# Kernel optimization log

Hardware: AMD Instinct MI355X
Metric: run time of the kernel (lower is better)

Reference implementation:

```python
import jax, jax.numpy as jnp
import numpy as np

NUM_HEADS = 16
HIDDEN = 1024
HEAD_DIM = HIDDEN // NUM_HEADS
B, L = 1, 2048


def setup_inputs() -> dict:
    key = jax.random.key(0)
    ks = jax.random.split(key, 5)
    scale = 1.0 / np.sqrt(HIDDEN)
    x = jax.random.normal(ks[0], (B, L, HIDDEN), dtype=jnp.float32)
    Wq = jax.random.normal(ks[1], (HIDDEN, HIDDEN), dtype=jnp.float32) * scale
    Wk = jax.random.normal(ks[2], (HIDDEN, HIDDEN), dtype=jnp.float32) * scale
    Wv = jax.random.normal(ks[3], (HIDDEN, HIDDEN), dtype=jnp.float32) * scale
    Wo = jax.random.normal(ks[4], (HIDDEN, HIDDEN), dtype=jnp.float32) * scale
    return {"x": x, "Wq": Wq, "Wk": Wk, "Wv": Wv, "Wo": Wo}


def reference(x, Wq, Wk, Wv, Wo):
    Bx, Lx, _ = x.shape
    # nn.Linear computes x @ W.T (bias=False)
    q = (x @ Wq.T).reshape(Bx, Lx, NUM_HEADS, HEAD_DIM)
    k = (x @ Wk.T).reshape(Bx, Lx, NUM_HEADS, HEAD_DIM)
    v = (x @ Wv.T).reshape(Bx, Lx, NUM_HEADS, HEAD_DIM)
    # elu(.)+1 feature map
    q = jax.nn.elu(q) + 1.0
    k = jax.nn.elu(k) + 1.0
    # causal linear-attention state via cumsum of kv outer products
    kv = jnp.einsum('blhd,blhe->blhde', k, v)           # [B,L,H,D,D]
    kv_cumsum = jnp.cumsum(kv, axis=1)
    k_cumsum = jnp.cumsum(k, axis=1)
    out = jnp.einsum('blhd,blhde->blhe', q, kv_cumsum)   # [B,L,H,D]
    denom = jnp.clip(jnp.einsum('blhd,blhd->blh', q, k_cumsum), 1e-6, None)
    out = out / denom[..., None]
    return out.reshape(Bx, Lx, HIDDEN) @ Wo.T
```

## Files before the change

### kernel.cpp

```cpp
#include <hip/hip_runtime.h>
#include <hip/hip_bf16.h>

typedef __attribute__((ext_vector_type(8))) short short8;
typedef __attribute__((ext_vector_type(4))) float floatx4;
typedef __attribute__((ext_vector_type(8))) unsigned short ushortx8;
typedef __attribute__((ext_vector_type(4))) unsigned short ushortx4;
typedef unsigned short u16;

#define HIDDEN 1024
#define NH 16
#define HD 64
#define SEQ 2048
#define CHUNK 128
#define NCHUNK (SEQ / CHUNK)

__device__ __forceinline__ u16 f2bf(float f) {
    union { float f; unsigned u; } v; v.f = f;
    unsigned r = v.u + 0x7fffu + ((v.u >> 16) & 1u);
    return (u16)(r >> 16);
}
__device__ __forceinline__ float bf2f(u16 u) {
    union { unsigned u; float f; } v; v.u = ((unsigned)u) << 16;
    return v.f;
}

__device__ __forceinline__ void gl_lds16(const u16* g, u16* l) {
    __builtin_amdgcn_global_load_lds(
        (const __attribute__((address_space(1))) void*)g,
        (__attribute__((address_space(3))) void*)l,
        16, 0, 0);
}

__global__ __launch_bounds__(256)
void convert_all(const float* __restrict__ x,  const float* __restrict__ Wq,
                 const float* __restrict__ Wk, const float* __restrict__ Wv,
                 const float* __restrict__ Wo,
                 u16* __restrict__ xb, u16* __restrict__ Wb, u16* __restrict__ Wob)
{
    const int total4 = 1572864;
    for (int idx = blockIdx.x * 256 + threadIdx.x; idx < total4; idx += gridDim.x * 256) {
        const float4* src; u16* dst; int off;
        if (idx < 524288)       { src = (const float4*)x;  dst = xb;            off = idx; }
        else if (idx < 786432)  { src = (const float4*)Wq; dst = Wb;            off = idx - 524288; }
        else if (idx < 1048576) { src = (const float4*)Wk; dst = Wb + 1048576;  off = idx - 786432; }
        else if (idx < 1310720) { src = (const float4*)Wv; dst = Wb + 2097152;  off = idx - 1048576; }
        else                    { src = (const float4*)Wo; dst = Wob;           off = idx - 1310720; }
        float4 v = src[off];
        ushortx4 u = { f2bf(v.x), f2bf(v.y), f2bf(v.z), f2bf(v.w) };
        *(ushortx4*)(dst + (size_t)off * 4) = u;
    }
}

__global__ __launch_bounds__(256, 3)
void qkv_gemm64(const u16* __restrict__ A, const u16* __restrict__ Bm,
                u16* __restrict__ qkb, u16* __restrict__ kT_b, u16* __restrict__ vT_b)
{
    __shared__ __align__(16) u16 smem[24576];
    auto As = (u16(*)[4096])smem;
    auto Bs = (u16(*)[8192])(smem + 8192);
    u16* Trow = smem;
    u16* Tcol = smem + 8704;

    const int L = blockIdx.x;
    const int xc = L & 7, i5 = L >> 3;
    const int m0 = (((xc >> 2) * 16) + (i5 & 15)) * 64;
    const int n0 = (((xc & 3) * 6) + (i5 >> 4)) * 128;

    const int t = threadIdx.x;
    const int lane = t & 63, wave = t >> 6;
    const int ln = lane & 15, q4 = lane >> 4;
    const int wm = (wave >> 1) * 32, wn = (wave & 1) * 64;
    const int r_in = t >> 3;
    const int csw = (((t & 7) ^ (r_in & 7)) << 3);

    const u16* Ag = A + (size_t)(m0 + r_in) * 1024 + csw;
    const u16* Bg = Bm + (size_t)(n0 + r_in) * 1024 + csw;

    floatx4 acc[2][4];
#pragma unroll
    for (int i = 0; i < 2; i++)
#pragma unroll
        for (int j = 0; j < 4; j++) acc[i][j] = (floatx4)0.0f;

    auto stage = [&](int buf, int k) {
        const int k0 = k * 64;
        gl_lds16(Ag + k0, &As[buf][t * 8]);
        gl_lds16(Ag + k0 + 32 * 1024, &As[buf][2048 + t * 8]);
#pragma unroll
        for (int i = 0; i < 4; i++)
            gl_lds16(Bg + k0 + (size_t)i * 32 * 1024, &Bs[buf][i * 2048 + t * 8]);
    };
    auto compute = [&](int buf) {
#pragma unroll
        for (int s = 0; s < 2; s++) {
            const int rc = (((s * 4 + q4) ^ (ln & 7)) << 3);
            short8 af[2], bfr[4];
#pragma unroll
            for (int i = 0; i < 2; i++)
                af[i] = *(const short8*)&As[buf][(wm + i * 16 + ln) * 64 + rc];
#pragma unroll
            for (int j = 0; j < 4; j++)
                bfr[j] = *(const short8*)&Bs[buf][(wn + j * 16 + ln) * 64 + rc];
#pragma unroll
            for (int i = 0; i < 2; i++)
#pragma unroll
                for (int j = 0; j < 4; j++)
                    acc[i][j] = __builtin_amdgcn_mfma_f32_16x16x32_bf16(af[i], bfr[j], acc[i][j], 0, 0, 0);
        }
    };

    stage(0, 0);
    stage(1, 1);
    for (int i = 0; i < 14; i++) {
        asm volatile("s_waitcnt vmcnt(6)" ::: "memory");
        __builtin_amdgcn_sched_barrier(0);
        __builtin_amdgcn_s_barrier();
        compute(i & 1);
        __builtin_amdgcn_sched_barrier(0);
        __builtin_amdgcn_s_barrier();
        stage(i & 1, i + 2);
    }
    asm volatile("s_waitcnt vmcnt(6)" ::: "memory");
    __builtin_amdgcn_sched_barrier(0);
    __builtin_amdgcn_s_barrier();
    compute(0);
    asm volatile("s_waitcnt vmcnt(0)" ::: "memory");
    __builtin_amdgcn_sched_barrier(0);
    __builtin_amdgcn_s_barrier();
    compute(1);

    __syncthreads();
    const int grp = n0 >> 10;
#pragma unroll
    for (int i = 0; i < 2; i++)
#pragma unroll
        for (int j = 0; j < 4; j++) {
            const int ml = wm + i * 16 + q4 * 4;
            const int nl = wn + j * 16 + ln;
            float vals[4];
#pragma unroll
            for (int r = 0; r < 4; r++) {
                float v = acc[i][j][r];
                if (grp < 2) v = (v > 0.f) ? (v + 1.f) : __expf(v);
                vals[r] = v;
            }
            if (grp < 2) {
#pragma unroll
                for (int r = 0; r < 4; r++) Trow[(ml + r) * 136 + nl] = f2bf(vals[r]);
            }
            if (grp >= 1) {
                ushortx4 u = { f2bf(vals[0]), f2bf(vals[1]), f2bf(vals[2]), f2bf(vals[3]) };
                *(ushortx4*)&Tcol[nl * 72 + ml] = u;
            }
        }
    __syncthreads();
    if (grp < 2) {
        const int ml = t >> 2, sg = (t & 3) * 32;
        const int col0 = (n0 & 1023) + (grp ? 1024 : 0) + sg;
        const u16* src = &Trow[ml * 136 + sg];
        u16* dst = &qkb[(size_t)(m0 + ml) * 2048 + col0];
#pragma unroll
        for (int p = 0; p < 4; p++)
            *(ushortx8*)&dst[p * 8] = *(const ushortx8*)&src[p * 8];
    }
    if (grp >= 1) {
        const int nl = t >> 1, sg = (t & 1) * 32;
        const int nh = (n0 & 1023) + nl;
        const u16* src = &Tcol[nl * 72 + sg];
        u16* dstb = (grp == 1) ? kT_b : vT_b;
        u16* dst = &dstb[(size_t)nh * 2048 + m0 + sg];
#pragma unroll
        for (int p = 0; p < 4; p++)
            *(ushortx8*)&dst[p * 8] = *(const ushortx8*)&src[p * 8];
    }
}

__global__ __launch_bounds__(256, 2)
void chunk_stats2(const u16* __restrict__ kT_b, const u16* __restrict__ vT_b,
                  float* __restrict__ S_ws, float* __restrict__ ksum_ws)
{
    __shared__ u16 kT_l[64 * 128];
    __shared__ u16 vT_l[64 * 128];
    const int c = blockIdx.x, h = blockIdx.y;
    const int t = threadIdx.x;
    const int lane = t & 63, w = t >> 6;
    const int ln = lane & 15, q4 = lane >> 4;
#pragma unroll
    for (int i = 0; i < 4; i++) {
        const int d0 = w * 16 + i * 4 + (lane >> 4);
        const int cc = lane & 15;
        const size_t gsrc = (size_t)(h * 64 + d0) * 2048 + c * 128 + ((cc ^ (d0 & 7)) << 3);
        gl_lds16(kT_b + gsrc, &kT_l[(w * 16 + i * 4) * 128 + lane * 8]);
        gl_lds16(vT_b + gsrc, &vT_l[(w * 16 + i * 4) * 128 + lane * 8]);
    }
    __syncthreads();
    floatx4 sacc[4];
#pragma unroll
    for (int j = 0; j < 4; j++) sacc[j] = (floatx4)0.0f;
#pragma unroll
    for (int ks = 0; ks < 4; ks++) {
        const int rc = (((ks * 4 + q4) ^ (ln & 7)) << 3);
        short8 af = *(const short8*)&kT_l[(w * 16 + ln) * 128 + rc];
#pragma unroll
        for (int j = 0; j < 4; j++) {
            short8 bfr = *(const short8*)&vT_l[(j * 16 + ln) * 128 + rc];
            sacc[j] = __builtin_amdgcn_mfma_f32_16x16x32_bf16(af, bfr, sacc[j], 0, 0, 0);
        }
    }
    float* Sp = S_ws + ((size_t)(h * NCHUNK + c) << 12);
#pragma unroll
    for (int j = 0; j < 4; j++)
#pragma unroll
        for (int r = 0; r < 4; r++) {
            int d = w * 16 + q4 * 4 + r;
            int e = j * 16 + ln;
            Sp[e * 64 + d] = sacc[j][r];
        }
    if (t < 64) {
        float s = 0.f;
#pragma unroll
        for (int cc = 0; cc < 16; cc++) {
            ushortx8 v8 = *(const ushortx8*)&kT_l[t * 128 + cc * 8];
#pragma unroll
            for (int jj = 0; jj < 8; jj++) s += bf2f(v8[jj]);
        }
        ksum_ws[(h * NCHUNK + c) * 64 + t] = s;
    }
}

__global__ __launch_bounds__(256)
void scan_kv(const float* __restrict__ S_ws, const float* __restrict__ ksum_ws,
             u16* __restrict__ kvpref_b, float* __restrict__ kspref)
{
    const int h = blockIdx.x, qt = blockIdx.y;
    const int t = threadIdx.x;
    const int li = qt * 1024 + t * 4;
    const int e = li >> 6, d0 = li & 63;
    const int slot = e * 64 + ((((d0 >> 3) ^ (e & 7)) << 3) | (d0 & 7));
    float a0 = 0.f, a1 = 0.f, a2 = 0.f, a3 = 0.f;
    for (int c = 0; c < 16; c++) {
        ushortx4 u = { f2bf(a0), f2bf(a1), f2bf(a2), f2bf(a3) };
        *(ushortx4*)&kvpref_b[(((size_t)(h * 16 + c)) << 12) + slot] = u;
        float4 s4 = *(const float4*)(S_ws + (((size_t)(h * 16 + c)) << 12) + li);
        a0 += s4.x; a1 += s4.y; a2 += s4.z; a3 += s4.w;
    }
    if (qt == 0 && t < 64) {
        float a = 0.f;
        for (int c = 0; c < 16; c++) {
            kspref[(h * 16 + c) * 64 + t] = a;
            a += ksum_ws[(h * 16 + c) * 64 + t];
        }
    }
}

__global__ __launch_bounds__(512, 2)
void attn_out2(const u16* __restrict__ qkb, const u16* __restrict__ vT_b,
               const u16* __restrict__ kvpref_b, const float* __restrict__ kspref,
               u16* __restrict__ attnb)
{
    __shared__ __align__(16) u16 smem[29824];
    u16* q_l   = smem;
    u16* k_l   = smem + 8192;
    u16* kvT_l = smem + 16384;
    u16* vT_l  = smem + 20480;
    u16* P_l   = smem;
    float* kpref  = (float*)(smem + 28672);
    float* denom4 = kpref + 64;

    const int c = blockIdx.x, h = blockIdx.y;
    const int t = threadIdx.x;
    const int lane = t & 63, w = t >> 6;
    const int ln = lane & 15, q4 = lane >> 4;

    {
        const int row = t >> 3, cc = t & 7;
        const size_t gq = (size_t)(c * CHUNK + row) * 2048 + h * 64
                        + (size_t)((cc ^ (row & 7)) << 3);
        gl_lds16(qkb + gq,        &q_l[t * 8]);
        gl_lds16(qkb + gq + 1024, &k_l[t * 8]);
        const int row2 = row + 64;
        const size_t gq2 = (size_t)(c * CHUNK + row2) * 2048 + h * 64
                         + (size_t)((cc ^ (row2 & 7)) << 3);
        gl_lds16(qkb + gq2,        &q_l[4096 + t * 8]);
        gl_lds16(qkb + gq2 + 1024, &k_l[4096 + t * 8]);
        const int d = t >> 4, cv = t & 15;
        gl_lds16(vT_b + (size_t)(h * 64 + d) * 2048 + c * 128 + ((cv ^ (d & 7)) << 3),
                 &vT_l[t * 8]);
        const int d2 = d + 32;
        gl_lds16(vT_b + (size_t)(h * 64 + d2) * 2048 + c * 128 + ((cv ^ (d2 & 7)) << 3),
                 &vT_l[4096 + t * 8]);
        gl_lds16(kvpref_b + (((size_t)(h * 16 + c)) << 12) + t * 8, &kvT_l[t * 8]);
    }
    if (t < 64) kpref[t] = kspref[(h * 16 + c) * 64 + t];
    __syncthreads();

    const int pm = (w >> 2) * 64, pn = (w & 3) * 32;
    floatx4 pacc[4][2];
#pragma unroll
    for (int i = 0; i < 4; i++)
#pragma unroll
        for (int j = 0; j < 2; j++) pacc[i][j] = (floatx4)0.0f;
#pragma unroll
    for (int s = 0; s < 2; s++) {
        const int rc = (((s * 4 + q4) ^ (ln & 7)) << 3);
        short8 af[4], bfr[2];
#pragma unroll
        for (int i = 0; i < 4; i++)
            af[i] = *(const short8*)&q_l[(pm + i * 16 + ln) * 64 + rc];
#pragma unroll
        for (int j = 0; j < 2; j++)
            bfr[j] = *(const short8*)&k_l[(pn + j * 16 + ln) * 64 + rc];
#pragma unroll
        for (int i = 0; i < 4; i++)
#pragma unroll
            for (int j = 0; j < 2; j++)
                pacc[i][j] = __builtin_amdgcn_mfma_f32_16x16x32_bf16(af[i], bfr[j], pacc[i][j], 0, 0, 0);
    }
#pragma unroll
    for (int i = 0; i < 4; i++)
#pragma unroll
        for (int r = 0; r < 4; r++) {
            int rowi = pm + i * 16 + q4 * 4 + r;
            float rs = 0.f;
#pragma unroll
            for (int j = 0; j < 2; j++) {
                int col = pn + j * 16 + ln;
                float p = pacc[i][j][r];
                if (col > rowi) p = 0.f;
                pacc[i][j][r] = p;
                rs += p;
            }
#pragma unroll
            for (int off = 1; off < 16; off <<= 1) rs += __shfl_xor(rs, off, 64);
            if (ln == 0) denom4[(w & 3) * 128 + rowi] = rs;
        }
    const int ob = w * 16;
    floatx4 oacc[4];
#pragma unroll
    for (int j = 0; j < 4; j++) oacc[j] = (floatx4)0.0f;
#pragma unroll
    for (int s = 0; s < 2; s++) {
        const int rc = (((s * 4 + q4) ^ (ln & 7)) << 3);
        short8 af = *(const short8*)&q_l[(ob + ln) * 64 + rc];
#pragma unroll
        for (int j = 0; j < 4; j++) {
            short8 bfr = *(const short8*)&kvT_l[(j * 16 + ln) * 64 + rc];
            oacc[j] = __builtin_amdgcn_mfma_f32_16x16x32_bf16(af, bfr, oacc[j], 0, 0, 0);
        }
    }
    __syncthreads();
    if (t < 128) {
        float s = 0.f;
#pragma unroll
        for (int c8 = 0; c8 < 8; c8++) {
            ushortx8 v8 = *(const ushortx8*)&q_l[t * 64 + ((c8 ^ (t & 7)) << 3)];
#pragma unroll
            for (int jj = 0; jj < 8; jj++) s += bf2f(v8[jj]) * kpref[c8 * 8 + jj];
        }
        denom4[t] += s;
    }
    __syncthreads();
#pragma unroll
    for (int i = 0; i < 4; i++)
#pragma unroll
        for (int j = 0; j < 2; j++)
#pragma unroll
            for (int r = 0; r < 4; r++) {
                int rowi = pm + i * 16 + q4 * 4 + r;
                int col = pn + j * 16 + ln;
                P_l[rowi * 136 + col] = f2bf(pacc[i][j][r]);
            }
    __syncthreads();
    for (int ks = 0; ks <= (w >> 1); ks++) {
        short8 af = *(const short8*)&P_l[(ob + ln) * 136 + ks * 32 + q4 * 8];
        const int rc = (((ks * 4 + q4) ^ (ln & 7)) << 3);
#pragma unroll
        for (int j = 0; j < 4; j++) {
            short8 bfr = *(const short8*)&vT_l[(j * 16 + ln) * 128 + rc];
            oacc[j] = __builtin_amdgcn_mfma_f32_16x16x32_bf16(af, bfr, oacc[j], 0, 0, 0);
        }
    }
#pragma unroll
    for (int r = 0; r < 4; r++) {
        const int rowi = ob + q4 * 4 + r;
        float den = denom4[rowi] + denom4[128 + rowi] + denom4[256 + rowi] + denom4[384 + rowi];
        den = fmaxf(den, 1e-6f);
#pragma unroll
        for (int j = 0; j < 4; j++) {
            int e = j * 16 + ln;
            attnb[(size_t)(c * CHUNK + rowi) * HIDDEN + h * HD + e] = f2bf(oacc[j][r] / den);
        }
    }
}

__global__ __launch_bounds__(256, 3)
void out_gemm64(const u16* __restrict__ A, const u16* __restrict__ Bm,
                float* __restrict__ out)
{
    __shared__ u16 As[2][64 * 64];
    __shared__ u16 Bs[2][64 * 64];
    const int L = blockIdx.x;
    const int xc = L & 7, i6 = L >> 3;
    const int m0 = (((xc >> 1) * 8) + (i6 & 7)) * 64;
    const int n0 = (((xc & 1) * 8) + (i6 >> 3)) * 64;
    const int t = threadIdx.x;
    const int lane = t & 63, wave = t >> 6;
    const int ln = lane & 15, q4 = lane >> 4;
    const int wm = (wave >> 1) * 32, wn = (wave & 1) * 32;
    const int r_in = t >> 3;
    const int csw = (((t & 7) ^ (r_in & 7)) << 3);

    const u16* Ag = A + (size_t)(m0 + r_in) * 1024 + csw;
    const u16* Bg = Bm + (size_t)(n0 + r_in) * 1024 + csw;

    floatx4 acc[2][2];
#pragma unroll
    for (int i = 0; i < 2; i++)
#pragma unroll
        for (int j = 0; j < 2; j++) acc[i][j] = (floatx4)0.0f;

    auto stage = [&](int buf, int k) {
        const int k0 = k * 64;
        gl_lds16(Ag + k0, &As[buf][t * 8]);
        gl_lds16(Ag + k0 + 32 * 1024, &As[buf][2048 + t * 8]);
        gl_lds16(Bg + k0, &Bs[buf][t * 8]);
        gl_lds16(Bg + k0 + 32 * 1024, &Bs[buf][2048 + t * 8]);
    };
    auto compute = [&](int buf) {
#pragma unroll
        for (int s = 0; s < 2; s++) {
            const int rc = (((s * 4 + q4) ^ (ln & 7)) << 3);
            short8 af[2], bfr[2];
#pragma unroll
            for (int i = 0; i < 2; i++)
                af[i] = *(const short8*)&As[buf][(wm + i * 16 + ln) * 64 + rc];
#pragma unroll
            for (int j = 0; j < 2; j++)
                bfr[j] = *(const short8*)&Bs[buf][(wn + j * 16 + ln) * 64 + rc];
#pragma unroll
            for (int i = 0; i < 2; i++)
#pragma unroll
                for (int j = 0; j < 2; j++)
                    acc[i][j] = __builtin_amdgcn_mfma_f32_16x16x32_bf16(af[i], bfr[j], acc[i][j], 0, 0, 0);
        }
    };

    stage(0, 0);
    stage(1, 1);
    for (int i = 0; i < 14; i++) {
        asm volatile("s_waitcnt vmcnt(4)" ::: "memory");
        __builtin_amdgcn_sched_barrier(0);
        __builtin_amdgcn_s_barrier();
        compute(i & 1);
        __builtin_amdgcn_sched_barrier(0);
        __builtin_amdgcn_s_barrier();
        stage(i & 1, i + 2);
    }
    asm volatile("s_waitcnt vmcnt(4)" ::: "memory");
    __builtin_amdgcn_sched_barrier(0);
    __builtin_amdgcn_s_barrier();
    compute(0);
    asm volatile("s_waitcnt vmcnt(0)" ::: "memory");
    __builtin_amdgcn_sched_barrier(0);
    __builtin_amdgcn_s_barrier();
    compute(1);

#pragma unroll
    for (int i = 0; i < 2; i++)
#pragma unroll
        for (int j = 0; j < 2; j++)
#pragma unroll
            for (int r = 0; r < 4; r++) {
                int m = m0 + wm + i * 16 + q4 * 4 + r;
                int n = n0 + wn + j * 16 + ln;
                out[(size_t)m * 1024 + n] = acc[i][j][r];
            }
}

extern "C" void kernel_launch(void* const* d_in, const int* in_sizes, int n_in,
                              void* d_out, int out_size, void* d_ws, size_t ws_size,
                              hipStream_t stream)
{
    const float* x  = (const float*)d_in[0];
    const float* Wq = (const float*)d_in[1];
    const float* Wk = (const float*)d_in[2];
    const float* Wv = (const float*)d_in[3];
    const float* Wo = (const float*)d_in[4];
    float* out = (float*)d_out;

    char* ws = (char*)d_ws;
    const size_t MB = 1024 * 1024;
    u16* xb    = (u16*)(ws);
    u16* Wb    = (u16*)(ws + 4 * MB);
    u16* Wob   = (u16*)(ws + 10 * MB);
    u16* qkb   = (u16*)(ws + 12 * MB);
    u16* kT_b  = (u16*)(ws + 20 * MB);
    u16* vT_b  = (u16*)(ws + 24 * MB);
    float* S_ws    = (float*)(ws + 28 * MB);
    float* ksum_ws = (float*)(ws + 32 * MB);
    u16* attnb = (u16*)(ws + 33 * MB);
    u16* kvpref_b = (u16*)(ws + 37 * MB);
    float* kspref = (float*)(ws + 39 * MB);

    convert_all<<<2048, 256, 0, stream>>>(x, Wq, Wk, Wv, Wo, xb, Wb, Wob);
    qkv_gemm64<<<768, 256, 0, stream>>>(xb, Wb, qkb, kT_b, vT_b);
    chunk_stats2<<<dim3(NCHUNK, NH), 256, 0, stream>>>(kT_b, vT_b, S_ws, ksum_ws);
    scan_kv<<<dim3(NH, 4), 256, 0, stream>>>(S_ws, ksum_ws, kvpref_b, kspref);
    attn_out2<<<dim3(NCHUNK, NH), 512, 0, stream>>>(qkb, vT_b, kvpref_b, kspref, attnb);
    out_gemm64<<<512, 256, 0, stream>>>(attnb, Wob, out);
}
```

Before: 127.8 us.

## Fuse chunk statistics and prefix scan into one double-buffered kernel; use nontemporal stores

Replaces the separate chunk_stats2 and scan_kv kernels with a single chunkscan kernel. Each block owns one head and a 16-column slice of e, walks all chunks sequentially with double-buffered LDS staging, and keeps the running KV prefix in registers. This removes the fp32 S_ws/ksum_ws round trip through global memory and one kernel launch. The cost is far less parallelism: 64 blocks instead of 256, each running a serial 16-step loop. Stores of qkb/kT/vT and the final output now use nontemporal hints.

```diff
diff --git a/kernel.cpp b/kernel.cpp
--- a/kernel.cpp
+++ b/kernel.cpp
@@ -161,7 +161,7 @@
         u16* dst = &qkb[(size_t)(m0 + ml) * 2048 + col0];
 #pragma unroll
         for (int p = 0; p < 4; p++)
-            *(ushortx8*)&dst[p * 8] = *(const ushortx8*)&src[p * 8];
+            __builtin_nontemporal_store(*(const ushortx8*)&src[p * 8], (ushortx8*)&dst[p * 8]);
     }
     if (grp >= 1) {
         const int nl = t >> 1, sg = (t & 1) * 32;
@@ -171,85 +171,74 @@
         u16* dst = &dstb[(size_t)nh * 2048 + m0 + sg];
 #pragma unroll
         for (int p = 0; p < 4; p++)
-            *(ushortx8*)&dst[p * 8] = *(const ushortx8*)&src[p * 8];
+            __builtin_nontemporal_store(*(const ushortx8*)&src[p * 8], (ushortx8*)&dst[p * 8]);
     }
 }
 
 __global__ __launch_bounds__(256, 2)
-void chunk_stats2(const u16* __restrict__ kT_b, const u16* __restrict__ vT_b,
-                  float* __restrict__ S_ws, float* __restrict__ ksum_ws)
-{
-    __shared__ u16 kT_l[64 * 128];
-    __shared__ u16 vT_l[64 * 128];
-    const int c = blockIdx.x, h = blockIdx.y;
+void chunkscan(const u16* __restrict__ kT_b, const u16* __restrict__ vT_b,
+               u16* __restrict__ kvpref_b, float* __restrict__ kspref)
+{
+    __shared__ u16 ktb[2][64 * 128];
+    __shared__ u16 vtb[2][16 * 128];
+    const int eq = blockIdx.x, h = blockIdx.y;
     const int t = threadIdx.x;
     const int lane = t & 63, w = t >> 6;
     const int ln = lane & 15, q4 = lane >> 4;
-#pragma unroll
-    for (int i = 0; i < 4; i++) {
-        const int d0 = w * 16 + i * 4 + (lane >> 4);
-        const int cc = lane & 15;
-        const size_t gsrc = (size_t)(h * 64 + d0) * 2048 + c * 128 + ((cc ^ (d0 & 7)) << 3);
-        gl_lds16(kT_b + gsrc, &kT_l[(w * 16 + i * 4) * 128 + lane * 8]);
-        gl_lds16(vT_b + gsrc, &vT_l[(w * 16 + i * 4) * 128 + lane * 8]);
-    }
-    __syncthreads();
-    floatx4 sacc[4];
-#pragma unroll
-    for (int j = 0; j < 4; j++) sacc[j] = (floatx4)0.0f;
-#pragma unroll
-    for (int ks = 0; ks < 4; ks++) {
-        const int rc = (((ks * 4 + q4) ^ (ln & 7)) << 3);
-        short8 af = *(const short8*)&kT_l[(w * 16 + ln) * 128 + rc];
-#pragma unroll
-        for (int j = 0; j < 4; j++) {
-            short8 bfr = *(const short8*)&vT_l[(j * 16 + ln) * 128 + rc];
-            sacc[j] = __builtin_amdgcn_mfma_f32_16x16x32_bf16(af, bfr, sacc[j], 0, 0, 0);
-        }
-    }
-    float* Sp = S_ws + ((size_t)(h * NCHUNK + c) << 12);
-#pragma unroll
-    for (int j = 0; j < 4; j++)
-#pragma unroll
-        for (int r = 0; r < 4; r++) {
-            int d = w * 16 + q4 * 4 + r;
-            int e = j * 16 + ln;
-            Sp[e * 64 + d] = sacc[j][r];
-        }
-    if (t < 64) {
-        float s = 0.f;
-#pragma unroll
-        for (int cc = 0; cc < 16; cc++) {
-            ushortx8 v8 = *(const ushortx8*)&kT_l[t * 128 + cc * 8];
-#pragma unroll
-            for (int jj = 0; jj < 8; jj++) s += bf2f(v8[jj]);
-        }
-        ksum_ws[(h * NCHUNK + c) * 64 + t] = s;
-    }
-}
-
-__global__ __launch_bounds__(256)
-void scan_kv(const float* __restrict__ S_ws, const float* __restrict__ ksum_ws,
-             u16* __restrict__ kvpref_b, float* __restrict__ kspref)
-{
-    const int h = blockIdx.x, qt = blockIdx.y;
-    const int t = threadIdx.x;
-    const int li = qt * 1024 + t * 4;
-    const int e = li >> 6, d0 = li & 63;
-    const int slot = e * 64 + ((((d0 >> 3) ^ (e & 7)) << 3) | (d0 & 7));
-    float a0 = 0.f, a1 = 0.f, a2 = 0.f, a3 = 0.f;
-    for (int c = 0; c < 16; c++) {
-        ushortx4 u = { f2bf(a0), f2bf(a1), f2bf(a2), f2bf(a3) };
-        *(ushortx4*)&kvpref_b[(((size_t)(h * 16 + c)) << 12) + slot] = u;
-        float4 s4 = *(const float4*)(S_ws + (((size_t)(h * 16 + c)) << 12) + li);
-        a0 += s4.x; a1 += s4.y; a2 += s4.z; a3 += s4.w;
-    }
-    if (qt == 0 && t < 64) {
-        float a = 0.f;
-        for (int c = 0; c < 16; c++) {
-            kspref[(h * 16 + c) * 64 + t] = a;
-            a += ksum_ws[(h * 16 + c) * 64 + t];
-        }
+
+    auto stageK = [&](int buf, int c) {
+#pragma unroll
+        for (int i = 0; i < 4; i++) {
+            const int d0 = w * 16 + i * 4 + (lane >> 4);
+            const int cc = lane & 15;
+            gl_lds16(kT_b + (size_t)(h * 64 + d0) * 2048 + c * 128 + ((cc ^ (d0 & 7)) << 3),
+                     &ktb[buf][(w * 16 + i * 4) * 128 + lane * 8]);
+        }
+    };
+    auto stageV = [&](int buf, int c) {
+        const int lr = t >> 4, cc = t & 15;
+        gl_lds16(vT_b + (size_t)(h * 64 + eq * 16 + lr) * 2048 + c * 128 + ((cc ^ (lr & 7)) << 3),
+                 &vtb[buf][t * 8]);
+    };
+
+    floatx4 pref = (floatx4)0.0f;
+    float ka = 0.f;
+
+    stageK(0, 0); stageV(0, 0);
+    __syncthreads();
+    int buf = 0;
+    for (int c = 0; c < NCHUNK; ++c) {
+        if (c < NCHUNK - 1) { stageK(buf ^ 1, c + 1); stageV(buf ^ 1, c + 1); }
+        floatx4 sacc = (floatx4)0.0f;
+#pragma unroll
+        for (int ks = 0; ks < 4; ks++) {
+            const int rc = (((ks * 4 + q4) ^ (ln & 7)) << 3);
+            short8 af = *(const short8*)&ktb[buf][(w * 16 + ln) * 128 + rc];
+            short8 bfr = *(const short8*)&vtb[buf][ln * 128 + rc];
+            sacc = __builtin_amdgcn_mfma_f32_16x16x32_bf16(af, bfr, sacc, 0, 0, 0);
+        }
+        {
+            const int d0 = w * 16 + q4 * 4;
+            const int e = eq * 16 + ln;
+            const int slot = e * 64 + ((((d0 >> 3) ^ (e & 7)) << 3) | (d0 & 7));
+            ushortx4 u = { f2bf(pref[0]), f2bf(pref[1]), f2bf(pref[2]), f2bf(pref[3]) };
+            *(ushortx4*)&kvpref_b[(((size_t)(h * 16 + c)) << 12) + slot] = u;
+        }
+#pragma unroll
+        for (int r = 0; r < 4; r++) pref[r] += sacc[r];
+        if (eq == 0 && t < 64) {
+            float s = 0.f;
+#pragma unroll
+            for (int cc = 0; cc < 16; cc++) {
+                ushortx8 v8 = *(const ushortx8*)&ktb[buf][t * 128 + cc * 8];
+#pragma unroll
+                for (int jj = 0; jj < 8; jj++) s += bf2f(v8[jj]);
+            }
+            kspref[(h * 16 + c) * 64 + t] = ka;
+            ka += s;
+        }
+        __syncthreads();
+        buf ^= 1;
     }
 }
 
@@ -473,7 +462,7 @@
             for (int r = 0; r < 4; r++) {
                 int m = m0 + wm + i * 16 + q4 * 4 + r;
                 int n = n0 + wn + j * 16 + ln;
-                out[(size_t)m * 1024 + n] = acc[i][j][r];
+                __builtin_nontemporal_store(acc[i][j][r], &out[(size_t)m * 1024 + n]);
             }
 }
 
@@ -496,16 +485,13 @@
     u16* qkb   = (u16*)(ws + 12 * MB);
     u16* kT_b  = (u16*)(ws + 20 * MB);
     u16* vT_b  = (u16*)(ws + 24 * MB);
-    float* S_ws    = (float*)(ws + 28 * MB);
-    float* ksum_ws = (float*)(ws + 32 * MB);
-    u16* attnb = (u16*)(ws + 33 * MB);
-    u16* kvpref_b = (u16*)(ws + 37 * MB);
-    float* kspref = (float*)(ws + 39 * MB);
+    u16* attnb = (u16*)(ws + 28 * MB);
+    u16* kvpref_b = (u16*)(ws + 32 * MB);
+    float* kspref = (float*)(ws + 34 * MB);
 
     convert_all<<<2048, 256, 0, stream>>>(x, Wq, Wk, Wv, Wo, xb, Wb, Wob);
     qkv_gemm64<<<768, 256, 0, stream>>>(xb, Wb, qkb, kT_b, vT_b);
-    chunk_stats2<<<dim3(NCHUNK, NH), 256, 0, stream>>>(kT_b, vT_b, S_ws, ksum_ws);
-    scan_kv<<<dim3(NH, 4), 256, 0, stream>>>(S_ws, ksum_ws, kvpref_b, kspref);
+    chunkscan<<<dim3(4, NH), 256, 0, stream>>>(kT_b, vT_b, kvpref_b, kspref);
     attn_out2<<<dim3(NCHUNK, NH), 512, 0, stream>>>(qkb, vT_b, kvpref_b, kspref, attnb);
     out_gemm64<<<512, 256, 0, stream>>>(attnb, Wob, out);
 }
```

Measured after the change: 153.3 us. 1.2x slower.
